# Kernel optimization log

Hardware: AMD Instinct MI355X
Metric: run time of the kernel (lower is better)

## Reference

```python
import jax, jax.numpy as jnp
import numpy as np

B, S, D, H = 64, 2048, 512, 512


def setup_inputs() -> dict:
    key = jax.random.key(0)
    ks = jax.random.split(key, 8)
    scale_in = 1.0 / np.sqrt(D)
    scale_v = 1.0 / np.sqrt(H)
    return {
        "x": jax.random.normal(ks[0], (B, D), jnp.float32),
        "context": jax.random.normal(ks[1], (B, S, D), jnp.float32),
        "mask": jax.random.randint(ks[2], (B, S), 0, 2).astype(bool),
        "W_in": jax.random.normal(ks[3], (H, D), jnp.float32) * scale_in,
        "b_in": jax.random.normal(ks[4], (H,), jnp.float32) * scale_in,
        "W_ctx": jax.random.normal(ks[5], (H, D), jnp.float32) * scale_in,
        "b_ctx": jax.random.normal(ks[6], (H,), jnp.float32) * scale_in,
        "V": jax.random.uniform(ks[7], (H,), jnp.float32, -scale_v, scale_v),
    }


def reference(x, context, mask, W_in, b_in, W_ctx, b_ctx, V):
    # inp: Linear(input) -> [B, H], broadcast over S
    inp = x @ W_in.T + b_in  # [B, H]
    # ctx: 1x1 Conv1d over permuted context == per-position linear -> [B, H, S]
    ctx = jnp.einsum("bsd,hd->bhs", context, W_ctx) + b_ctx[None, :, None]
    # additive (Bahdanau) scores: V . tanh(inp + ctx) -> [B, S]
    att = jnp.einsum("h,bhs->bs", V, jnp.tanh(inp[:, :, None] + ctx))
    # mask selected positions with -inf, softmax over seq dim
    att = jnp.where(mask, -jnp.inf, att)
    alpha = jax.nn.softmax(att, axis=1)  # [B, S]
    # weighted sum of ctx columns -> [B, H]
    hidden_state = jnp.einsum("bhs,bs->bh", ctx, alpha)
    return hidden_state, alpha
```

## Files before the change

### kernel.cpp

```cpp
#include <hip/hip_runtime.h>
#include <hip/hip_bf16.h>
#include <cstdint>

#define B_ 64
#define S_ 2048
#define D_ 512
#define H_ 512

typedef short s16x8 __attribute__((ext_vector_type(8)));
typedef float f32x4 __attribute__((ext_vector_type(4)));

static __device__ __forceinline__ unsigned short f2bf(float f) {
  __bf16 h = (__bf16)f;
  return __builtin_bit_cast(unsigned short, h);
}

__global__ __launch_bounds__(256) void k_prep(
    const unsigned int* __restrict__ mw, int* __restrict__ flags,
    const float* __restrict__ W, unsigned short* __restrict__ Wp,
    const float* __restrict__ x, const float* __restrict__ W_in,
    const float* __restrict__ b_in, const float* __restrict__ b_ctx,
    float* __restrict__ inp_pb) {
  const int bx = blockIdx.x;
  const int t = threadIdx.x;
  if (bx < 128) {
    __shared__ int blk;
    if (t == 0) blk = 0;
    __syncthreads();
    unsigned w = mw[bx * 256 + t];
    int bits = 0;
    if (w == 0x3F800000u) bits = 2;
    else if (w > 1u) bits = 1;
    unsigned long long a1 = __ballot(bits & 1);
    unsigned long long a2 = __ballot(bits & 2);
    if ((t & 63) == 0) {
      int v = (a1 ? 1 : 0) | (a2 ? 2 : 0);
      if (v) atomicOr(&blk, v);
    }
    __syncthreads();
    if (t == 0) flags[bx] = blk;
  } else if (bx < 256) {
    const int tid = (bx - 128) * 256 + t;
    const int lane = tid & 63;
    const int hb = (tid >> 6) & 31;
    const int kb = tid >> 11;
    const int h = hb * 16 + (lane & 15);
    const int k = kb * 32 + (lane >> 4) * 8;
    const float* src = W + (size_t)h * D_ + k;
    float4 a = *(const float4*)src;
    float4 c = *(const float4*)(src + 4);
    s16x8 o;
    o[0] = (short)f2bf(a.x); o[1] = (short)f2bf(a.y);
    o[2] = (short)f2bf(a.z); o[3] = (short)f2bf(a.w);
    o[4] = (short)f2bf(c.x); o[5] = (short)f2bf(c.y);
    o[6] = (short)f2bf(c.z); o[7] = (short)f2bf(c.w);
    *(s16x8*)(Wp + (size_t)tid * 8) = o;
  } else {
    const int b = bx - 256;
    __shared__ float xs[D_];
    xs[t] = x[b * D_ + t];
    xs[t + 256] = x[b * D_ + t + 256];
    __syncthreads();
    for (int h = t; h < H_; h += 256) {
      const float4* wr = (const float4*)(W_in + (size_t)h * D_);
      float acc = 0.f;
#pragma unroll 4
      for (int d4 = 0; d4 < 128; ++d4) {
        float4 w = wr[d4];
        acc += w.x * xs[d4 * 4] + w.y * xs[d4 * 4 + 1] + w.z * xs[d4 * 4 + 2] +
               w.w * xs[d4 * 4 + 3];
      }
      inp_pb[b * H_ + h] = acc + b_in[h] + b_ctx[h];
    }
  }
}

__global__ __launch_bounds__(512, 2) void k_att(
    const float* __restrict__ context, const unsigned short* __restrict__ Wp,
    const float* __restrict__ inp_pb, const float* __restrict__ V,
    float* __restrict__ att) {
  __shared__ char bt[2][8192];
  __shared__ float red[8][64];
  const int tid = threadIdx.x;
  const int wave = tid >> 6, lane = tid & 63;
  const int b = blockIdx.y, s0 = blockIdx.x * 64;
  const float* ctxb = context + ((size_t)b * S_ + s0) * D_;
  const int hbase = wave * 64;
  const int bln = lane & 15, blh = lane >> 4;

  const int srow = tid >> 3, kc8 = (tid & 7) * 8;
  const int sbyte = srow * 128 + ((kc8 * 2) ^ ((srow & 7) << 4));
  const float* gsrc = ctxb + (size_t)srow * D_ + kc8;

  const unsigned short* ap = Wp + ((size_t)(wave * 4) * 64 + lane) * 8;

  f32x4 acc[4][4];
#pragma unroll
  for (int m = 0; m < 4; ++m)
#pragma unroll
    for (int n = 0; n < 4; ++n) acc[m][n] = f32x4{0.f, 0.f, 0.f, 0.f};

  f32x4 sg0a, sg0b, sg1a, sg1b, sg2a, sg2b;
#define LOAD_SET0(T) { sg0a = __builtin_nontemporal_load((const f32x4*)(gsrc + (T)*64)); \
                       sg0b = __builtin_nontemporal_load((const f32x4*)(gsrc + (T)*64 + 4)); }
#define LOAD_SET1(T) { sg1a = __builtin_nontemporal_load((const f32x4*)(gsrc + (T)*64)); \
                       sg1b = __builtin_nontemporal_load((const f32x4*)(gsrc + (T)*64 + 4)); }
#define LOAD_SET2(T) { sg2a = __builtin_nontemporal_load((const f32x4*)(gsrc + (T)*64)); \
                       sg2b = __builtin_nontemporal_load((const f32x4*)(gsrc + (T)*64 + 4)); }
#define CVT_SET(A, Bv, BUF) { s16x8 hb_; \
    hb_[0] = (short)f2bf((A)[0]); hb_[1] = (short)f2bf((A)[1]); \
    hb_[2] = (short)f2bf((A)[2]); hb_[3] = (short)f2bf((A)[3]); \
    hb_[4] = (short)f2bf((Bv)[0]); hb_[5] = (short)f2bf((Bv)[1]); \
    hb_[6] = (short)f2bf((Bv)[2]); hb_[7] = (short)f2bf((Bv)[3]); \
    *(s16x8*)(&bt[BUF][sbyte]) = hb_; }

  LOAD_SET0(0);
  LOAD_SET1(1);
  LOAD_SET2(2);
  CVT_SET(sg0a, sg0b, 0);
  asm volatile("s_waitcnt lgkmcnt(0)" ::: "memory");
  __builtin_amdgcn_s_barrier();
  __builtin_amdgcn_sched_barrier(0);

#pragma unroll
  for (int t = 0; t < 8; ++t) {
    const char* cur = bt[t & 1];
    s16x8 bfrag[2][4];
#pragma unroll
    for (int kk = 0; kk < 2; ++kk)
#pragma unroll
      for (int n = 0; n < 4; ++n) {
        const int sr = n * 16 + bln;
        const int off = (kk * 64 + blh * 16) ^ ((sr & 7) << 4);
        bfrag[kk][n] = *(const s16x8*)(cur + sr * 128 + off);
      }
    s16x8 af[2][4];
#pragma unroll
    for (int kk = 0; kk < 2; ++kk)
#pragma unroll
      for (int m = 0; m < 4; ++m)
        af[kk][m] = *(const s16x8*)(ap + (size_t)(t * 2 + kk) * 32 * 512 +
                                    (size_t)m * 512);
    if (t < 5) {
      const int s3 = (t + 3) % 3;
      if (s3 == 0) LOAD_SET0(t + 3)
      else if (s3 == 1) LOAD_SET1(t + 3)
      else LOAD_SET2(t + 3)
    }
    __builtin_amdgcn_s_setprio(1);
#pragma unroll
    for (int kk = 0; kk < 2; ++kk)
#pragma unroll
      for (int m = 0; m < 4; ++m)
#pragma unroll
        for (int n = 0; n < 4; ++n)
          acc[m][n] = __builtin_amdgcn_mfma_f32_16x16x32_bf16(af[kk][m],
                                                              bfrag[kk][n],
                                                              acc[m][n], 0, 0, 0);
    __builtin_amdgcn_s_setprio(0);
    if (t < 7) {
      const int s1 = (t + 1) % 3;
      const int nb = (t + 1) & 1;
      if (s1 == 0) CVT_SET(sg0a, sg0b, nb)
      else if (s1 == 1) CVT_SET(sg1a, sg1b, nb)
      else CVT_SET(sg2a, sg2b, nb)
    }
    asm volatile("s_waitcnt lgkmcnt(0)" ::: "memory");
    __builtin_amdgcn_s_barrier();
    __builtin_amdgcn_sched_barrier(0);
  }
#undef LOAD_SET0
#undef LOAD_SET1
#undef LOAD_SET2
#undef CVT_SET

  float attp[4] = {0.f, 0.f, 0.f, 0.f};
  const float* ib = inp_pb + b * H_;
#pragma unroll
  for (int m = 0; m < 4; ++m) {
#pragma unroll
    for (int j = 0; j < 4; ++j) {
      int h = hbase + m * 16 + (blh << 2) + j;
      float c = ib[h];
      float vh = V[h];
#pragma unroll
      for (int n = 0; n < 4; ++n) {
        float x = acc[m][n][j] + c;
        float ax = __builtin_fabsf(x);
        float e = __expf(2.f * ax);
        float tt = 1.f - 2.f * __builtin_amdgcn_rcpf(e + 1.f);
        attp[n] += vh * copysignf(tt, x);
      }
    }
  }
#pragma unroll
  for (int n = 0; n < 4; ++n) {
    attp[n] += __shfl_xor(attp[n], 16, 64);
    attp[n] += __shfl_xor(attp[n], 32, 64);
  }
  if (lane < 16) {
#pragma unroll
    for (int n = 0; n < 4; ++n) red[wave][n * 16 + lane] = attp[n];
  }
  __syncthreads();
  if (tid < 64) {
    float s = 0.f;
#pragma unroll
    for (int w = 0; w < 8; ++w) s += red[w][tid];
    att[(size_t)b * S_ + s0 + tid] = s;
  }
}

__global__ void k_softmax(const float* __restrict__ att, const void* __restrict__ mask,
                          const int* __restrict__ flags, float* __restrict__ alpha) {
  const int b = blockIdx.x, t = threadIdx.x;
  __shared__ int cshared;
  __shared__ float sm[4];
  if (t < 64) {
    int v = flags[t] | flags[t + 64];
    for (int off = 32; off; off >>= 1) v |= __shfl_xor(v, off, 64);
    if (t == 0) cshared = v;
  }
  __syncthreads();
  const int c = cshared;
  const int mtype = (c & 2) ? 2 : (c & 1);
  const unsigned char* m8 = (const unsigned char*)mask;
  const int* m32 = (const int*)mask;
  const float* mf = (const float*)mask;
  float vals[8];
  float mx = -3.0e38f;
#pragma unroll
  for (int i = 0; i < 8; ++i) {
    int s = t + i * 256;
    size_t idx = (size_t)b * S_ + s;
    int msk = (mtype == 1) ? (int)m8[idx] : (mtype == 2) ? (mf[idx] != 0.f) : m32[idx];
    float v = msk ? -__builtin_inff() : att[idx];
    vals[i] = v;
    mx = fmaxf(mx, v);
  }
  for (int off = 32; off; off >>= 1) mx = fmaxf(mx, __shfl_xor(mx, off, 64));
  if ((t & 63) == 0) sm[t >> 6] = mx;
  __syncthreads();
  mx = fmaxf(fmaxf(sm[0], sm[1]), fmaxf(sm[2], sm[3]));
  float es[8];
  float sum = 0.f;
#pragma unroll
  for (int i = 0; i < 8; ++i) {
    es[i] = __expf(vals[i] - mx);
    sum += es[i];
  }
  for (int off = 32; off; off >>= 1) sum += __shfl_xor(sum, off, 64);
  __syncthreads();
  if ((t & 63) == 0) sm[t >> 6] = sum;
  __syncthreads();
  sum = sm[0] + sm[1] + sm[2] + sm[3];
  float inv = __fdividef(1.f, sum);
#pragma unroll
  for (int i = 0; i < 8; ++i) alpha[(size_t)b * S_ + t + i * 256] = es[i] * inv;
}

__global__ void k_ypart(const float* __restrict__ context,
                        const float* __restrict__ alpha, float* __restrict__ y_part) {
  const int chunk = blockIdx.x, b = blockIdx.y, t = threadIdx.x;
  __shared__ float al[256];
  __shared__ float4 part[128];
  al[t] = alpha[(size_t)b * S_ + chunk * 256 + t];
  __syncthreads();
  const int d4 = t & 127, sr = t >> 7;
  const float4* base = (const float4*)(context + ((size_t)b * S_ + chunk * 256) * D_);
  float4 acc = make_float4(0.f, 0.f, 0.f, 0.f);
  for (int i = 0; i < 128; ++i) {
    int s = sr + 2 * i;
    float4 v = base[(size_t)s * 128 + d4];
    float a = al[s];
    acc.x += a * v.x; acc.y += a * v.y; acc.z += a * v.z; acc.w += a * v.w;
  }
  if (sr == 1) part[d4] = acc;
  __syncthreads();
  if (sr == 0) {
    float4 o = part[d4];
    o.x += acc.x; o.y += acc.y; o.z += acc.z; o.w += acc.w;
    *(float4*)(y_part + ((size_t)(b * 8 + chunk)) * D_ + d4 * 4) = o;
  }
}

__global__ void k_hidden(const float* __restrict__ y_part, const float* __restrict__ W_ctx,
                         const float* __restrict__ b_ctx, float* __restrict__ hidden) {
  const int b = blockIdx.x, t = threadIdx.x;
  __shared__ float ys[D_];
  for (int d = t; d < D_; d += 256) {
    float s = 0.f;
#pragma unroll
    for (int c = 0; c < 8; ++c) s += y_part[((size_t)(b * 8 + c)) * D_ + d];
    ys[d] = s;
  }
  __syncthreads();
  for (int h = t; h < H_; h += 256) {
    const float4* wr = (const float4*)(W_ctx + (size_t)h * D_);
    float acc = 0.f;
#pragma unroll 4
    for (int d4 = 0; d4 < 128; ++d4) {
      float4 w = wr[d4];
      acc += w.x * ys[d4 * 4] + w.y * ys[d4 * 4 + 1] + w.z * ys[d4 * 4 + 2] +
             w.w * ys[d4 * 4 + 3];
    }
    hidden[b * H_ + h] = acc + b_ctx[h];
  }
}

extern "C" void kernel_launch(void* const* d_in, const int* in_sizes, int n_in,
                              void* d_out, int out_size, void* d_ws, size_t ws_size,
                              hipStream_t stream) {
  (void)in_sizes; (void)n_in; (void)out_size; (void)ws_size;
  const float* x = (const float*)d_in[0];
  const float* context = (const float*)d_in[1];
  const void* mask = d_in[2];
  const float* W_in = (const float*)d_in[3];
  const float* b_in = (const float*)d_in[4];
  const float* W_ctx = (const float*)d_in[5];
  const float* b_ctx = (const float*)d_in[6];
  const float* V = (const float*)d_in[7];

  float* out_hidden = (float*)d_out;
  float* out_alpha = (float*)d_out + B_ * H_;

  char* ws = (char*)d_ws;
  float* inp_pb = (float*)ws;
  float* att = (float*)(ws + 131072);
  float* y_part = (float*)(ws + 655360);
  int* flags = (int*)(ws + 1703936);
  unsigned short* Wp = (unsigned short*)(ws + 1704448);

  k_prep<<<320, 256, 0, stream>>>((const unsigned int*)mask, flags, W_ctx, Wp,
                                  x, W_in, b_in, b_ctx, inp_pb);
  k_att<<<dim3(S_ / 64, B_), 512, 0, stream>>>(context, Wp, inp_pb, V, att);
  k_softmax<<<B_, 256, 0, stream>>>(att, mask, flags, out_alpha);
  k_ypart<<<dim3(8, B_), 256, 0, stream>>>(context, out_alpha, y_part);
  k_hidden<<<B_, 256, 0, stream>>>(y_part, W_ctx, b_ctx, out_hidden);
}
```

Baseline: 226.8 us.

## Write bf16 copy of context in attention kernel and reuse it for weighted sum

During the attention-score pass, the bf16-converted context tiles are also stored to a workspace buffer. The later weighted-sum kernel then reads this half-size bf16 copy instead of re-reading the fp32 context, halving that pass's read traffic. In exchange, the attention kernel gains an extra 128 MB of writes, and the weighted sum now runs on bf16-rounded context values. The path is taken only when the workspace is big enough, with the fp32 kernel kept as a fallback.

```diff
diff --git a/kernel.cpp b/kernel.cpp
--- a/kernel.cpp
+++ b/kernel.cpp
@@ -9,10 +9,15 @@
 
 typedef short s16x8 __attribute__((ext_vector_type(8)));
 typedef float f32x4 __attribute__((ext_vector_type(4)));
+typedef unsigned short u16x8 __attribute__((ext_vector_type(8)));
 
 static __device__ __forceinline__ unsigned short f2bf(float f) {
   __bf16 h = (__bf16)f;
   return __builtin_bit_cast(unsigned short, h);
+}
+static __device__ __forceinline__ float bf2f(unsigned short u) {
+  unsigned int w = ((unsigned int)u) << 16;
+  return __builtin_bit_cast(float, w);
 }
 
 __global__ __launch_bounds__(256) void k_prep(
@@ -78,7 +83,7 @@
 __global__ __launch_bounds__(512, 2) void k_att(
     const float* __restrict__ context, const unsigned short* __restrict__ Wp,
     const float* __restrict__ inp_pb, const float* __restrict__ V,
-    float* __restrict__ att) {
+    float* __restrict__ att, unsigned short* __restrict__ ctx16) {
   __shared__ char bt[2][8192];
   __shared__ float red[8][64];
   const int tid = threadIdx.x;
@@ -91,6 +96,8 @@
   const int srow = tid >> 3, kc8 = (tid & 7) * 8;
   const int sbyte = srow * 128 + ((kc8 * 2) ^ ((srow & 7) << 4));
   const float* gsrc = ctxb + (size_t)srow * D_ + kc8;
+  unsigned short* gdst = ctx16 ? ctx16 + ((size_t)b * S_ + s0 + srow) * D_ + kc8
+                               : (unsigned short*)0;
 
   const unsigned short* ap = Wp + ((size_t)(wave * 4) * 64 + lane) * 8;
 
@@ -107,17 +114,18 @@
                        sg1b = __builtin_nontemporal_load((const f32x4*)(gsrc + (T)*64 + 4)); }
 #define LOAD_SET2(T) { sg2a = __builtin_nontemporal_load((const f32x4*)(gsrc + (T)*64)); \
                        sg2b = __builtin_nontemporal_load((const f32x4*)(gsrc + (T)*64 + 4)); }
-#define CVT_SET(A, Bv, BUF) { s16x8 hb_; \
+#define CVT_SET(A, Bv, BUF, T) { s16x8 hb_; \
     hb_[0] = (short)f2bf((A)[0]); hb_[1] = (short)f2bf((A)[1]); \
     hb_[2] = (short)f2bf((A)[2]); hb_[3] = (short)f2bf((A)[3]); \
     hb_[4] = (short)f2bf((Bv)[0]); hb_[5] = (short)f2bf((Bv)[1]); \
     hb_[6] = (short)f2bf((Bv)[2]); hb_[7] = (short)f2bf((Bv)[3]); \
-    *(s16x8*)(&bt[BUF][sbyte]) = hb_; }
+    *(s16x8*)(&bt[BUF][sbyte]) = hb_; \
+    if (gdst) __builtin_nontemporal_store(hb_, (s16x8*)(gdst + (T) * 64)); }
 
   LOAD_SET0(0);
   LOAD_SET1(1);
   LOAD_SET2(2);
-  CVT_SET(sg0a, sg0b, 0);
+  CVT_SET(sg0a, sg0b, 0, 0);
   asm volatile("s_waitcnt lgkmcnt(0)" ::: "memory");
   __builtin_amdgcn_s_barrier();
   __builtin_amdgcn_sched_barrier(0);
@@ -161,9 +169,9 @@
     if (t < 7) {
       const int s1 = (t + 1) % 3;
       const int nb = (t + 1) & 1;
-      if (s1 == 0) CVT_SET(sg0a, sg0b, nb)
-      else if (s1 == 1) CVT_SET(sg1a, sg1b, nb)
-      else CVT_SET(sg2a, sg2b, nb)
+      if (s1 == 0) CVT_SET(sg0a, sg0b, nb, t + 1)
+      else if (s1 == 1) CVT_SET(sg1a, sg1b, nb, t + 1)
+      else CVT_SET(sg2a, sg2b, nb, t + 1)
     }
     asm volatile("s_waitcnt lgkmcnt(0)" ::: "memory");
     __builtin_amdgcn_s_barrier();
@@ -259,8 +267,43 @@
   for (int i = 0; i < 8; ++i) alpha[(size_t)b * S_ + t + i * 256] = es[i] * inv;
 }
 
-__global__ void k_ypart(const float* __restrict__ context,
-                        const float* __restrict__ alpha, float* __restrict__ y_part) {
+__global__ __launch_bounds__(256) void k_ypart16(const unsigned short* __restrict__ ctx16,
+                                                 const float* __restrict__ alpha,
+                                                 float* __restrict__ y_part) {
+  const int chunk = blockIdx.x, b = blockIdx.y, t = threadIdx.x;
+  const int g = t >> 6, lane = t & 63;
+  __shared__ float al[256];
+  __shared__ float part[3][512];
+  al[t] = alpha[(size_t)b * S_ + chunk * 256 + t];
+  __syncthreads();
+  float a8[8];
+#pragma unroll
+  for (int j = 0; j < 8; ++j) a8[j] = 0.f;
+  const unsigned short* base = ctx16 + ((size_t)b * S_ + chunk * 256) * D_ + lane * 8;
+  for (int i = 0; i < 64; ++i) {
+    int s = g * 64 + i;
+    u16x8 v = *(const u16x8*)(base + (size_t)s * D_);
+    float a = al[s];
+#pragma unroll
+    for (int j = 0; j < 8; ++j) a8[j] += a * bf2f(v[j]);
+  }
+  if (g > 0) {
+#pragma unroll
+    for (int j = 0; j < 8; ++j) part[g - 1][lane * 8 + j] = a8[j];
+  }
+  __syncthreads();
+  if (g == 0) {
+#pragma unroll
+    for (int j = 0; j < 8; ++j) {
+      float s = a8[j] + part[0][lane * 8 + j] + part[1][lane * 8 + j] +
+                part[2][lane * 8 + j];
+      y_part[((size_t)(b * 8 + chunk)) * D_ + lane * 8 + j] = s;
+    }
+  }
+}
+
+__global__ void k_ypart_f32(const float* __restrict__ context,
+                            const float* __restrict__ alpha, float* __restrict__ y_part) {
   const int chunk = blockIdx.x, b = blockIdx.y, t = threadIdx.x;
   __shared__ float al[256];
   __shared__ float4 part[128];
@@ -311,7 +354,7 @@
 extern "C" void kernel_launch(void* const* d_in, const int* in_sizes, int n_in,
                               void* d_out, int out_size, void* d_ws, size_t ws_size,
                               hipStream_t stream) {
-  (void)in_sizes; (void)n_in; (void)out_size; (void)ws_size;
+  (void)in_sizes; (void)n_in; (void)out_size;
   const float* x = (const float*)d_in[0];
   const float* context = (const float*)d_in[1];
   const void* mask = d_in[2];
@@ -330,11 +373,19 @@
   float* y_part = (float*)(ws + 655360);
   int* flags = (int*)(ws + 1703936);
   unsigned short* Wp = (unsigned short*)(ws + 1704448);
+  unsigned short* ctx16 = (unsigned short*)(ws + 2228736);
+  const size_t need = 2228736 + (size_t)B_ * S_ * D_ * 2;
+  const bool big_ws = (ws_size >= need);
 
   k_prep<<<320, 256, 0, stream>>>((const unsigned int*)mask, flags, W_ctx, Wp,
                                   x, W_in, b_in, b_ctx, inp_pb);
-  k_att<<<dim3(S_ / 64, B_), 512, 0, stream>>>(context, Wp, inp_pb, V, att);
+  k_att<<<dim3(S_ / 64, B_), 512, 0, stream>>>(context, Wp, inp_pb, V, att,
+                                               big_ws ? ctx16 : (unsigned short*)0);
   k_softmax<<<B_, 256, 0, stream>>>(att, mask, flags, out_alpha);
-  k_ypart<<<dim3(8, B_), 256, 0, stream>>>(context, out_alpha, y_part);
+  if (big_ws) {
+    k_ypart16<<<dim3(8, B_), 256, 0, stream>>>(ctx16, out_alpha, y_part);
+  } else {
+    k_ypart_f32<<<dim3(8, B_), 256, 0, stream>>>(context, out_alpha, y_part);
+  }
   k_hidden<<<B_, 256, 0, stream>>>(y_part, W_ctx, b_ctx, out_hidden);
 }
```

Result: slower. 241.4 us (+6.4%).

## Pre-pack context into bf16 MFMA fragment layout and reuse it for weighted sum

Applied to the files above, without the earlier changes.

Adds a packing kernel that converts the fp32 context into bf16, laid out in MFMA B-fragment order. The attention GEMM then loads fragments straight from global memory, with no LDS staging, barriers or in-kernel conversion. The weighted-sum kernel reads the packed bf16 copy instead of fp32 context, halving its traffic but lowering the precision of the hidden-state path. The cost is an extra full pass that reads fp32 and writes a 128MB bf16 buffer, which must fit in the workspace.

```diff
diff --git a/kernel.cpp b/kernel.cpp
--- a/kernel.cpp
+++ b/kernel.cpp
@@ -9,10 +9,15 @@
 
 typedef short s16x8 __attribute__((ext_vector_type(8)));
 typedef float f32x4 __attribute__((ext_vector_type(4)));
+typedef unsigned short u16x8 __attribute__((ext_vector_type(8)));
 
 static __device__ __forceinline__ unsigned short f2bf(float f) {
   __bf16 h = (__bf16)f;
   return __builtin_bit_cast(unsigned short, h);
+}
+static __device__ __forceinline__ float bf2f(unsigned short u) {
+  unsigned int w = ((unsigned int)u) << 16;
+  return __builtin_bit_cast(float, w);
 }
 
 __global__ __launch_bounds__(256) void k_prep(
@@ -75,24 +80,42 @@
   }
 }
 
-__global__ __launch_bounds__(512, 2) void k_att(
-    const float* __restrict__ context, const unsigned short* __restrict__ Wp,
+__global__ __launch_bounds__(256) void k_packctx(const float* __restrict__ ctx,
+                                                 unsigned short* __restrict__ Bp) {
+  const int tid = blockIdx.x * 256 + threadIdx.x;
+  const int lane = tid & 63;
+  const int q = tid >> 6;
+  const int n = q & 3;
+  const int kb = (q >> 2) & 15;
+  const int st = (q >> 6) & 31;
+  const int b = q >> 11;
+  const int s = st * 64 + n * 16 + (lane & 15);
+  const int k = kb * 32 + (lane >> 4) * 8;
+  const float* src = ctx + ((size_t)b * S_ + s) * D_ + k;
+  float4 a = *(const float4*)src;
+  float4 c = *(const float4*)(src + 4);
+  s16x8 o;
+  o[0] = (short)f2bf(a.x); o[1] = (short)f2bf(a.y);
+  o[2] = (short)f2bf(a.z); o[3] = (short)f2bf(a.w);
+  o[4] = (short)f2bf(c.x); o[5] = (short)f2bf(c.y);
+  o[6] = (short)f2bf(c.z); o[7] = (short)f2bf(c.w);
+  __builtin_nontemporal_store(o, (s16x8*)(Bp + (size_t)tid * 8));
+}
+
+__global__ __launch_bounds__(512, 4) void k_att(
+    const unsigned short* __restrict__ Bp, const unsigned short* __restrict__ Wp,
     const float* __restrict__ inp_pb, const float* __restrict__ V,
     float* __restrict__ att) {
-  __shared__ char bt[2][8192];
   __shared__ float red[8][64];
   const int tid = threadIdx.x;
   const int wave = tid >> 6, lane = tid & 63;
-  const int b = blockIdx.y, s0 = blockIdx.x * 64;
-  const float* ctxb = context + ((size_t)b * S_ + s0) * D_;
+  const int st = blockIdx.x, b = blockIdx.y;
+  const int s0 = st * 64;
   const int hbase = wave * 64;
-  const int bln = lane & 15, blh = lane >> 4;
-
-  const int srow = tid >> 3, kc8 = (tid & 7) * 8;
-  const int sbyte = srow * 128 + ((kc8 * 2) ^ ((srow & 7) << 4));
-  const float* gsrc = ctxb + (size_t)srow * D_ + kc8;
+  const int blh = lane >> 4;
 
   const unsigned short* ap = Wp + ((size_t)(wave * 4) * 64 + lane) * 8;
+  const unsigned short* bp = Bp + (size_t)(b * 32 + st) * 32768 + (size_t)lane * 8;
 
   f32x4 acc[4][4];
 #pragma unroll
@@ -100,79 +123,22 @@
 #pragma unroll
     for (int n = 0; n < 4; ++n) acc[m][n] = f32x4{0.f, 0.f, 0.f, 0.f};
 
-  f32x4 sg0a, sg0b, sg1a, sg1b, sg2a, sg2b;
-#define LOAD_SET0(T) { sg0a = __builtin_nontemporal_load((const f32x4*)(gsrc + (T)*64)); \
-                       sg0b = __builtin_nontemporal_load((const f32x4*)(gsrc + (T)*64 + 4)); }
-#define LOAD_SET1(T) { sg1a = __builtin_nontemporal_load((const f32x4*)(gsrc + (T)*64)); \
-                       sg1b = __builtin_nontemporal_load((const f32x4*)(gsrc + (T)*64 + 4)); }
-#define LOAD_SET2(T) { sg2a = __builtin_nontemporal_load((const f32x4*)(gsrc + (T)*64)); \
-                       sg2b = __builtin_nontemporal_load((const f32x4*)(gsrc + (T)*64 + 4)); }
-#define CVT_SET(A, Bv, BUF) { s16x8 hb_; \
-    hb_[0] = (short)f2bf((A)[0]); hb_[1] = (short)f2bf((A)[1]); \
-    hb_[2] = (short)f2bf((A)[2]); hb_[3] = (short)f2bf((A)[3]); \
-    hb_[4] = (short)f2bf((Bv)[0]); hb_[5] = (short)f2bf((Bv)[1]); \
-    hb_[6] = (short)f2bf((Bv)[2]); hb_[7] = (short)f2bf((Bv)[3]); \
-    *(s16x8*)(&bt[BUF][sbyte]) = hb_; }
-
-  LOAD_SET0(0);
-  LOAD_SET1(1);
-  LOAD_SET2(2);
-  CVT_SET(sg0a, sg0b, 0);
-  asm volatile("s_waitcnt lgkmcnt(0)" ::: "memory");
-  __builtin_amdgcn_s_barrier();
-  __builtin_amdgcn_sched_barrier(0);
-
-#pragma unroll
-  for (int t = 0; t < 8; ++t) {
-    const char* cur = bt[t & 1];
-    s16x8 bfrag[2][4];
-#pragma unroll
-    for (int kk = 0; kk < 2; ++kk)
-#pragma unroll
-      for (int n = 0; n < 4; ++n) {
-        const int sr = n * 16 + bln;
-        const int off = (kk * 64 + blh * 16) ^ ((sr & 7) << 4);
-        bfrag[kk][n] = *(const s16x8*)(cur + sr * 128 + off);
-      }
-    s16x8 af[2][4];
-#pragma unroll
-    for (int kk = 0; kk < 2; ++kk)
-#pragma unroll
-      for (int m = 0; m < 4; ++m)
-        af[kk][m] = *(const s16x8*)(ap + (size_t)(t * 2 + kk) * 32 * 512 +
-                                    (size_t)m * 512);
-    if (t < 5) {
-      const int s3 = (t + 3) % 3;
-      if (s3 == 0) LOAD_SET0(t + 3)
-      else if (s3 == 1) LOAD_SET1(t + 3)
-      else LOAD_SET2(t + 3)
-    }
-    __builtin_amdgcn_s_setprio(1);
-#pragma unroll
-    for (int kk = 0; kk < 2; ++kk)
-#pragma unroll
-      for (int m = 0; m < 4; ++m)
-#pragma unroll
-        for (int n = 0; n < 4; ++n)
-          acc[m][n] = __builtin_amdgcn_mfma_f32_16x16x32_bf16(af[kk][m],
-                                                              bfrag[kk][n],
-                                                              acc[m][n], 0, 0, 0);
-    __builtin_amdgcn_s_setprio(0);
-    if (t < 7) {
-      const int s1 = (t + 1) % 3;
-      const int nb = (t + 1) & 1;
-      if (s1 == 0) CVT_SET(sg0a, sg0b, nb)
-      else if (s1 == 1) CVT_SET(sg1a, sg1b, nb)
-      else CVT_SET(sg2a, sg2b, nb)
-    }
-    asm volatile("s_waitcnt lgkmcnt(0)" ::: "memory");
-    __builtin_amdgcn_s_barrier();
-    __builtin_amdgcn_sched_barrier(0);
-  }
-#undef LOAD_SET0
-#undef LOAD_SET1
-#undef LOAD_SET2
-#undef CVT_SET
+#pragma unroll
+  for (int kb = 0; kb < 16; ++kb) {
+    s16x8 af[4], bf[4];
+#pragma unroll
+    for (int m = 0; m < 4; ++m)
+      af[m] = *(const s16x8*)(ap + (size_t)(kb * 32 + m) * 512);
+#pragma unroll
+    for (int n = 0; n < 4; ++n)
+      bf[n] = *(const s16x8*)(bp + (size_t)(kb * 4 + n) * 512);
+#pragma unroll
+    for (int m = 0; m < 4; ++m)
+#pragma unroll
+      for (int n = 0; n < 4; ++n)
+        acc[m][n] = __builtin_amdgcn_mfma_f32_16x16x32_bf16(af[m], bf[n],
+                                                            acc[m][n], 0, 0, 0);
+  }
 
   float attp[4] = {0.f, 0.f, 0.f, 0.f};
   const float* ib = inp_pb + b * H_;
@@ -259,41 +225,45 @@
   for (int i = 0; i < 8; ++i) alpha[(size_t)b * S_ + t + i * 256] = es[i] * inv;
 }
 
-__global__ void k_ypart(const float* __restrict__ context,
-                        const float* __restrict__ alpha, float* __restrict__ y_part) {
-  const int chunk = blockIdx.x, b = blockIdx.y, t = threadIdx.x;
-  __shared__ float al[256];
-  __shared__ float4 part[128];
-  al[t] = alpha[(size_t)b * S_ + chunk * 256 + t];
-  __syncthreads();
-  const int d4 = t & 127, sr = t >> 7;
-  const float4* base = (const float4*)(context + ((size_t)b * S_ + chunk * 256) * D_);
-  float4 acc = make_float4(0.f, 0.f, 0.f, 0.f);
-  for (int i = 0; i < 128; ++i) {
-    int s = sr + 2 * i;
-    float4 v = base[(size_t)s * 128 + d4];
-    float a = al[s];
-    acc.x += a * v.x; acc.y += a * v.y; acc.z += a * v.z; acc.w += a * v.w;
-  }
-  if (sr == 1) part[d4] = acc;
-  __syncthreads();
-  if (sr == 0) {
-    float4 o = part[d4];
-    o.x += acc.x; o.y += acc.y; o.z += acc.z; o.w += acc.w;
-    *(float4*)(y_part + ((size_t)(b * 8 + chunk)) * D_ + d4 * 4) = o;
-  }
-}
-
-__global__ void k_hidden(const float* __restrict__ y_part, const float* __restrict__ W_ctx,
+__global__ __launch_bounds__(256) void k_ypart16f(const unsigned short* __restrict__ Bp,
+                                                  const float* __restrict__ alpha,
+                                                  float* __restrict__ y) {
+  const int kb = blockIdx.x, b = blockIdx.y, t = threadIdx.x;
+  const int wave = t >> 6, lane = t & 63;
+  const int sl = lane & 15;
+  __shared__ float comb[256][8];
+  float a8[8];
+#pragma unroll
+  for (int j = 0; j < 8; ++j) a8[j] = 0.f;
+  const float* al = alpha + (size_t)b * S_;
+  for (int st = wave * 8; st < wave * 8 + 8; ++st) {
+#pragma unroll
+    for (int n = 0; n < 4; ++n) {
+      const size_t fi = ((((size_t)(b * 32 + st) * 16 + kb) * 4 + n) * 64 + lane) * 8;
+      u16x8 v = *(const u16x8*)(Bp + fi);
+      float a = al[st * 64 + n * 16 + sl];
+#pragma unroll
+      for (int j = 0; j < 8; ++j) a8[j] += a * bf2f(v[j]);
+    }
+  }
+#pragma unroll
+  for (int j = 0; j < 8; ++j) comb[t][j] = a8[j];
+  __syncthreads();
+  if (t < 32) {
+    const int kh = t >> 3, e = t & 7;
+    float s = 0.f;
+#pragma unroll
+    for (int w = 0; w < 4; ++w)
+      for (int s2 = 0; s2 < 16; ++s2) s += comb[w * 64 + kh * 16 + s2][e];
+    y[(size_t)b * D_ + kb * 32 + t] = s;
+  }
+}
+
+__global__ void k_hidden(const float* __restrict__ y, const float* __restrict__ W_ctx,
                          const float* __restrict__ b_ctx, float* __restrict__ hidden) {
   const int b = blockIdx.x, t = threadIdx.x;
   __shared__ float ys[D_];
-  for (int d = t; d < D_; d += 256) {
-    float s = 0.f;
-#pragma unroll
-    for (int c = 0; c < 8; ++c) s += y_part[((size_t)(b * 8 + c)) * D_ + d];
-    ys[d] = s;
-  }
+  for (int d = t; d < D_; d += 256) ys[d] = y[(size_t)b * D_ + d];
   __syncthreads();
   for (int h = t; h < H_; h += 256) {
     const float4* wr = (const float4*)(W_ctx + (size_t)h * D_);
@@ -327,14 +297,16 @@
   char* ws = (char*)d_ws;
   float* inp_pb = (float*)ws;
   float* att = (float*)(ws + 131072);
-  float* y_part = (float*)(ws + 655360);
-  int* flags = (int*)(ws + 1703936);
-  unsigned short* Wp = (unsigned short*)(ws + 1704448);
+  float* y = (float*)(ws + 655360);
+  int* flags = (int*)(ws + 786432);
+  unsigned short* Wp = (unsigned short*)(ws + 786944);
+  unsigned short* Bp = (unsigned short*)(ws + 1311232);
 
   k_prep<<<320, 256, 0, stream>>>((const unsigned int*)mask, flags, W_ctx, Wp,
                                   x, W_in, b_in, b_ctx, inp_pb);
-  k_att<<<dim3(S_ / 64, B_), 512, 0, stream>>>(context, Wp, inp_pb, V, att);
+  k_packctx<<<32768, 256, 0, stream>>>(context, Bp);
+  k_att<<<dim3(S_ / 64, B_), 512, 0, stream>>>(Bp, Wp, inp_pb, V, att);
   k_softmax<<<B_, 256, 0, stream>>>(att, mask, flags, out_alpha);
-  k_ypart<<<dim3(8, B_), 256, 0, stream>>>(context, out_alpha, y_part);
-  k_hidden<<<B_, 256, 0, stream>>>(y_part, W_ctx, b_ctx, out_hidden);
-}
+  k_ypart16f<<<dim3(16, B_), 256, 0, stream>>>(Bp, out_alpha, y);
+  k_hidden<<<B_, 256, 0, stream>>>(y, W_ctx, b_ctx, out_hidden);
+}
```

Measured after the change: 283.6 us. 25.1% more time.
